# Kernel tuning notes

Measured on AMD Instinct MI355X. Metric: run time of the kernel, lower is better.

## Reference

```python
import jax, jax.numpy as jnp
import numpy as np

N = 50000       # nodes per batched graph
E = 800000      # edges per batched graph
G = 256         # graphs per batch (for max-node pooling)
VOCAB = 120     # node types == embedding vocab
D_EMB = 32
D_H = 100
D_FC = 32
MIN_TYPE = 5    # min_type_count in compute_node_pair_mmd
CAP = 25        # max_nodes_per_type (deterministic: first CAP nodes per type)
KER_MUL = 2.0   # standard multi-kernel Gaussian MMD settings
KER_NUM = 5


def setup_inputs() -> dict:
    key = jax.random.key(0)
    ks = jax.random.split(key, 16)
    ri = lambda k, sh, hi: jax.random.randint(k, sh, 0, hi, dtype=jnp.int32)
    feat = ri(ks[0], (N,), VOCAB)
    feat_src = ri(ks[1], (N,), VOCAB)
    feat_tar = ri(ks[2], (N,), VOCAB)
    edge_index = ri(ks[3], (2, E), N)
    edge_index_src = ri(ks[4], (2, E), N)
    edge_index_tar = ri(ks[5], (2, E), N)
    graph_ids = (jnp.arange(N, dtype=jnp.int32) * G) // N  # sorted, even partition
    mask = (jax.random.uniform(ks[6], (N,)) > 0.1).astype(jnp.float32)
    embed = jax.random.normal(ks[7], (VOCAB, D_EMB)) * 0.02
    gcn_w = jax.random.normal(ks[8], (D_EMB, D_H)) * (1.0 / np.sqrt(D_EMB))
    gcn_b = jnp.zeros((D_H,), jnp.float32)
    fc_w = jax.random.normal(ks[9], (D_H, D_FC)) * (1.0 / np.sqrt(D_H))
    fc_b = jnp.zeros((D_FC,), jnp.float32)
    def_w = jax.random.normal(ks[10], (D_FC, 1)) * (1.0 / np.sqrt(D_FC))
    def_b = jnp.zeros((1,), jnp.float32)
    return dict(feat=feat, feat_src=feat_src, feat_tar=feat_tar,
                edge_index=edge_index, edge_index_src=edge_index_src,
                edge_index_tar=edge_index_tar, graph_ids=graph_ids, mask=mask,
                embed=embed, gcn_w=gcn_w, gcn_b=gcn_b, fc_w=fc_w, fc_b=fc_b,
                def_w=def_w, def_b=def_b)


def _graph_conv(x, ei, w, b):
    # DGL GraphConv, norm='both': D_out^{-1/2} A^T D_in^{-1/2} X W + b (degrees clamped to 1)
    src, dst = ei[0], ei[1]
    ones = jnp.ones((ei.shape[1],), x.dtype)
    outdeg = jnp.clip(jax.ops.segment_sum(ones, src, num_segments=N), 1.0)
    indeg = jnp.clip(jax.ops.segment_sum(ones, dst, num_segments=N), 1.0)
    h = (x @ w) * (outdeg ** -0.5)[:, None]          # [N, D_H], weight first (in<=out)
    agg = jax.ops.segment_sum(h[src], dst, num_segments=N)
    return agg * (indeg ** -0.5)[:, None] + b


def _mmd(src_types, tgt_types, src_feats, tgt_feats):
    # per-type multi-kernel Gaussian MMD; deterministic cap of CAP nodes/type
    def per_type(t):
        sm = (src_types == t)
        tm = (tgt_types == t)
        s_cnt = sm.sum()
        t_cnt = tm.sum()
        sv, si = jax.lax.top_k(sm.astype(jnp.float32), CAP)  # first CAP indices of type t
        tv, ti = jax.lax.top_k(tm.astype(jnp.float32), CAP)
        X = jnp.concatenate([src_feats[si], tgt_feats[ti]], 0)      # [2C, D]
        valid = jnp.concatenate([sv, tv]) > 0                        # [2C]
        pm = valid[:, None] & valid[None, :]
        D2 = jnp.sum((X[:, None, :] - X[None, :, :]) ** 2, -1)      # [2C, 2C]
        m = jnp.minimum(s_cnt, CAP).astype(jnp.float32)
        n = jnp.minimum(t_cnt, CAP).astype(jnp.float32)
        ntot = m + n
        bw = jnp.sum(jnp.where(pm, D2, 0.0)) / jnp.maximum(ntot * ntot - ntot, 1.0)
        bw = bw / (KER_MUL ** (KER_NUM // 2))
        bws = bw * (KER_MUL ** jnp.arange(KER_NUM, dtype=jnp.float32))
        K = jnp.sum(jnp.exp(-D2[None] / jnp.maximum(bws, 1e-8)[:, None, None]), 0)
        K = jnp.where(pm, K, 0.0)
        XX = K[:CAP, :CAP].sum() / jnp.maximum(m * m, 1.0)
        YY = K[CAP:, CAP:].sum() / jnp.maximum(n * n, 1.0)
        XY = K[:CAP, CAP:].sum() / jnp.maximum(m * n, 1.0)
        loss = XX + YY - 2.0 * XY
        inc = (s_cnt >= MIN_TYPE) & (t_cnt >= MIN_TYPE)
        return jnp.where(inc, loss, 0.0), inc.astype(jnp.float32)
    losses, incs = jax.vmap(per_type)(jnp.arange(1, VOCAB, dtype=jnp.int32))  # type 0 skipped
    cnt = incs.sum()
    return jnp.where(cnt > 0, losses.sum() / jnp.maximum(cnt, 1.0), 0.0)


def reference(feat, feat_src, feat_tar, edge_index, edge_index_src, edge_index_tar,
              graph_ids, mask, embed, gcn_w, gcn_b, fc_w, fc_b, def_w, def_b):
    def process(f, ei, msk):
        x = embed[f]
        if msk is not None:
            x = x * msk[:, None]
        h = jax.nn.relu(_graph_conv(x, ei, gcn_w, gcn_b))            # node feats 'h'
        pooled = jax.ops.segment_max(h, graph_ids, num_segments=G,
                                     indices_are_sorted=True)        # dgl.max_nodes
        return h, pooled

    _, pool = process(feat, edge_index, mask)
    h_src, pool_src = process(feat_src, edge_index_src, None)
    h_tar, pool_tar = process(feat_tar, edge_index_tar, None)

    x_batch_mmd = pool @ fc_w + fc_b        # [G, 32]
    x_src_mmd = pool_src @ fc_w + fc_b
    x_tar_mmd = pool_tar @ fc_w + fc_b
    src_node_feat = h_src @ fc_w + fc_b     # [N, 32]
    tgt_node_feat = h_tar @ fc_w + fc_b
    x_loss_mmd_node = _mmd(feat_src, feat_tar, src_node_feat, tgt_node_feat)
    defect_prob = jax.nn.sigmoid(x_batch_mmd @ def_w + def_b)  # [G, 1]
    # domain_clf output is not returned by the original forward, so it is skipped here.
    return (x_batch_mmd, defect_prob, x_src_mmd, x_tar_mmd, x_loss_mmd_node)
```

## Files before the change

### kernel.cpp

```cpp
#include <hip/hip_runtime.h>
#include <hip/hip_bf16.h>

#define Nn 50000
#define Ee 800000
#define Gg 256
#define VOC 120
#define DH 100
#define CAPc 25
#define NTYPE 119
#define NCHUNK 196
#define DR 4
#define DS 32
#define DWORDS 6250
#define NBIN 391
#define EBLK 782

#define P1_T 0
#define P1_SEL 120
#define P1_BIN 512
#define P1_DEG 2858
#define P1_PCLR 3242
#define P1_SCLR 3317
#define P1_TOT 3415
#define P2_SELP 0
#define P2_BINP 240
#define P2_DMG 1413
#define P2_TOT 2585
#define P3_SELG 0
#define P3_BSC 392
#define P3_TOT 2738

__global__ __launch_bounds__(256) void prep_kernel(
        const float* __restrict__ embed, const float* __restrict__ gcn_w, float* __restrict__ Tp,
        const int* __restrict__ feat_src, const int* __restrict__ feat_tar,
        int* __restrict__ chunkcnt,
        const int* __restrict__ ei0, const int* __restrict__ ei1, const int* __restrict__ ei2,
        int* __restrict__ cntbuf, int* __restrict__ partial,
        float* __restrict__ pool, int* __restrict__ selpos, float* __restrict__ stats) {
    __shared__ int sm[DWORDS];
    int bx = blockIdx.x;
    int tid = threadIdx.x;

    if (bx < P1_SEL) {
        int t = bx - P1_T;
        if (tid < DH) {
            float acc = 0.f;
#pragma unroll
            for (int k = 0; k < 32; ++k) acc = fmaf(embed[t * 32 + k], gcn_w[k * DH + tid], acc);
            Tp[t * DH + tid] = acc;
        }
        return;
    }
    if (bx < P1_BIN) {
        int idx = bx - P1_SEL;
        int side = idx / NCHUNK, chunk = idx - side * NCHUNK;
        const int* f = side ? feat_tar : feat_src;
        if (tid < VOC) sm[tid] = 0;
        __syncthreads();
        int i = chunk * 256 + tid;
        if (i < Nn) atomicAdd(&sm[f[i]], 1);
        __syncthreads();
        if (tid < VOC) chunkcnt[(side * NCHUNK + chunk) * VOC + tid] = sm[tid];
        return;
    }
    if (bx < P1_DEG) {
        int idx = bx - P1_BIN;
        int g = idx / EBLK, blk = idx - g * EBLK;
        const int* dst = ((g == 0) ? ei0 : (g == 1) ? ei1 : ei2) + Ee;
        for (int i = tid; i < NBIN; i += 256) sm[i] = 0;
        __syncthreads();
        int e0 = (blk * 256 + tid) * 4;
        if (e0 < Ee) {
            uint4 d = *(const uint4*)&dst[e0];
            atomicAdd(&sm[d.x >> 7], 1);
            atomicAdd(&sm[d.y >> 7], 1);
            atomicAdd(&sm[d.z >> 7], 1);
            atomicAdd(&sm[d.w >> 7], 1);
        }
        __syncthreads();
        int* outp = cntbuf + ((size_t)blk * 3 + g) * NBIN;
        for (int i = tid; i < NBIN; i += 256) outp[i] = sm[i];
        return;
    }
    if (bx < P1_PCLR) {
        int idx = bx - P1_DEG;
        int g = idx / (DR * DS), rs = idx - g * (DR * DS);
        int r = rs & (DR - 1), s = rs >> 2;
        const int* ei = (g == 0) ? ei0 : (g == 1) ? ei1 : ei2;
        const uint4* a4 = (const uint4*)(ei + s * (Ee / DS));
        for (int i = tid; i < DWORDS; i += 256) sm[i] = 0;
        __syncthreads();
        unsigned base = r * (2 * DWORDS);
        for (int idx2 = tid; idx2 < (Ee / DS) / 4; idx2 += 256) {
            uint4 v = a4[idx2];
            unsigned q;
            q = v.x - base; if (q < 2 * DWORDS) atomicAdd(&sm[q >> 1], 1 << ((q & 1) * 16));
            q = v.y - base; if (q < 2 * DWORDS) atomicAdd(&sm[q >> 1], 1 << ((q & 1) * 16));
            q = v.z - base; if (q < 2 * DWORDS) atomicAdd(&sm[q >> 1], 1 << ((q & 1) * 16));
            q = v.w - base; if (q < 2 * DWORDS) atomicAdd(&sm[q >> 1], 1 << ((q & 1) * 16));
        }
        __syncthreads();
        int* outp = partial + ((size_t)(g * DR + r) * DS + s) * DWORDS;
        for (int i = tid; i < DWORDS; i += 256) outp[i] = sm[i];
        return;
    }
    if (bx < P1_SCLR) {
        int i = (bx - P1_PCLR) * 256 + tid;
        ((float4*)pool)[i] = make_float4(0.f, 0.f, 0.f, 0.f);
        return;
    }
    {
        int b = bx - P1_SCLR;
        int i = b * 256 + tid;
        if (i < 25000) ((int4*)selpos)[i] = make_int4(-1, -1, -1, -1);
        if (b == 0 && tid == 0) {
            stats[0] = 0.f;
            ((int*)stats)[1] = 0;
            ((int*)stats)[2] = 0;
        }
        return;
    }
}

__global__ __launch_bounds__(64) void prefix_kernel(const int* __restrict__ chunkcnt,
                                                    int* __restrict__ baseb,
                                                    int* __restrict__ fullcnt,
                                                    const int* __restrict__ cntbuf,
                                                    int* __restrict__ ofsbuf,
                                                    int* __restrict__ bintot,
                                                    const int* __restrict__ partial,
                                                    const int* __restrict__ feat0,
                                                    const int* __restrict__ feat_src,
                                                    const int* __restrict__ feat_tar,
                                                    const float* __restrict__ mask,
                                                    float2* __restrict__ pc) {
    int bx = blockIdx.x;
    int lane = threadIdx.x;
    if (bx < P2_BINP) {
        int side = bx / VOC, t = bx - side * VOC;
        int run = 0;
        for (int c0 = 0; c0 < NCHUNK; c0 += 64) {
            int c = c0 + lane;
            int v = (c < NCHUNK) ? chunkcnt[(side * NCHUNK + c) * VOC + t] : 0;
            int inc = v;
#pragma unroll
            for (int o = 1; o < 64; o <<= 1) {
                int u = __shfl_up(inc, o, 64);
                if (lane >= o) inc += u;
            }
            if (c < NCHUNK) baseb[(side * NCHUNK + c) * VOC + t] = run + inc - v;
            run += __shfl(inc, 63, 64);
        }
        if (lane == 0) fullcnt[side * VOC + t] = run;
        return;
    }
    if (bx < P2_DMG) {
        int pair = bx - P2_BINP;
        int g = pair / NBIN, bin = pair - g * NBIN;
        int run = 0;
        for (int c0 = 0; c0 < EBLK; c0 += 64) {
            int c = c0 + lane;
            int v = (c < EBLK) ? cntbuf[((size_t)c * 3 + g) * NBIN + bin] : 0;
            int inc = v;
#pragma unroll
            for (int o = 1; o < 64; o <<= 1) {
                int u = __shfl_up(inc, o, 64);
                if (lane >= o) inc += u;
            }
            if (c < EBLK) ofsbuf[((size_t)c * 3 + g) * NBIN + bin] = run + inc - v;
            run += __shfl(inc, 63, 64);
        }
        if (lane == 0) bintot[pair] = run;
        return;
    }
    {
        int idx = (bx - P2_DMG) * 64 + lane;
        if (idx >= 3 * DR * DWORDS) return;
        int g = idx / (DR * DWORDS);
        int rem = idx - g * (DR * DWORDS);
        int r = rem / DWORDS, w = rem - r * DWORDS;
        const int* p = partial + ((size_t)(g * DR + r) * DS) * DWORDS + w;
        int sum = 0;
#pragma unroll 8
        for (int s = 0; s < DS; ++s) sum += p[s * DWORDS];
        int c0 = sum & 0xFFFF, c1 = sum >> 16;
        int n0 = r * (2 * DWORDS) + 2 * w;
        const int* ft = (g == 0) ? feat0 : (g == 1) ? feat_src : feat_tar;
        float cf0 = rsqrtf((float)max(c0, 1));
        float cf1 = rsqrtf((float)max(c1, 1));
        if (g == 0) {
            cf0 *= mask[n0];
            cf1 *= mask[n0 + 1];
        }
        float4 v = make_float4(cf0, __int_as_float(ft[n0]), cf1, __int_as_float(ft[n0 + 1]));
        ((float4*)(pc + (size_t)g * Nn))[r * DWORDS + w] = v;
        return;
    }
}

__global__ __launch_bounds__(64) void binbase_kernel(const int* __restrict__ bintot,
                                                     int* __restrict__ binbase) {
    int g = blockIdx.x;
    int lane = threadIdx.x;
    int run = 0;
    for (int c0 = 0; c0 < NBIN; c0 += 64) {
        int c = c0 + lane;
        int v = (c < NBIN) ? bintot[g * NBIN + c] : 0;
        int inc = v;
#pragma unroll
        for (int o = 1; o < 64; o <<= 1) {
            int u = __shfl_up(inc, o, 64);
            if (lane >= o) inc += u;
        }
        if (c < NBIN) binbase[g * NBIN + c] = run + inc - v;
        run += __shfl(inc, 63, 64);
    }
}

__global__ __launch_bounds__(256) void scatter_kernel(
        const int* __restrict__ feat_src, const int* __restrict__ feat_tar,
        const int* __restrict__ baseb, int* __restrict__ selpos_src, int* __restrict__ selpos_tar,
        const int* __restrict__ ei0, const int* __restrict__ ei1, const int* __restrict__ ei2,
        const int* __restrict__ ofsbuf, const int* __restrict__ binbase,
        uint2* __restrict__ ebuf, const float2* __restrict__ pc) {
    __shared__ int sm[NBIN];
    int bx = blockIdx.x;
    int tid = threadIdx.x;

    if (bx < P3_BSC) {
        int idx = bx - P3_SELG;
        int side = idx / NCHUNK, chunk = idx - side * NCHUNK;
        const int* f = side ? feat_tar : feat_src;
        int* selpos = side ? selpos_tar : selpos_src;
        int i = chunk * 256 + tid;
        int t = (i < Nn) ? f[i] : -1;
        sm[tid] = t;
        int bv = 0;
        bool need = (t >= 1);
        if (need) {
            bv = baseb[(side * NCHUNK + chunk) * VOC + t];
            need = (bv < CAPc);
        }
        int any = __syncthreads_count((int)need);
        if (any == 0) return;
        if (need) {
            int rank = bv;
            for (int q = 0; q < 256; ++q)
                if (q < tid && sm[q] == t) rank++;
            if (rank < CAPc) selpos[i] = (t - 1) * CAPc + rank;
        }
        return;
    }
    {
        int idx = bx - P3_BSC;
        int g = idx / EBLK, blk = idx - g * EBLK;
        const int* ei = (g == 0) ? ei0 : (g == 1) ? ei1 : ei2;
        const int* ofp = ofsbuf + ((size_t)blk * 3 + g) * NBIN;
        for (int i = tid; i < NBIN; i += 256)
            sm[i] = binbase[g * NBIN + i] + ofp[i];
        __syncthreads();
        const float2* pcg = pc + (size_t)g * Nn;
        uint2* eb = ebuf + (size_t)g * Ee;
        int e0 = (blk * 256 + tid) * 4;
        if (e0 < Ee) {
            uint4 s = *(const uint4*)&ei[e0];
            uint4 d = *(const uint4*)&ei[Ee + e0];
            float2 p0 = pcg[s.x];
            float2 p1 = pcg[s.y];
            float2 p2 = pcg[s.z];
            float2 p3 = pcg[s.w];
            int p;
            p = atomicAdd(&sm[d.x >> 7], 1);
            eb[p] = make_uint2(__float_as_uint(p0.x), __float_as_int(p0.y) * 128 + (d.x & 127u));
            p = atomicAdd(&sm[d.y >> 7], 1);
            eb[p] = make_uint2(__float_as_uint(p1.x), __float_as_int(p1.y) * 128 + (d.y & 127u));
            p = atomicAdd(&sm[d.z >> 7], 1);
            eb[p] = make_uint2(__float_as_uint(p2.x), __float_as_int(p2.y) * 128 + (d.z & 127u));
            p = atomicAdd(&sm[d.w >> 7], 1);
            eb[p] = make_uint2(__float_as_uint(p3.x), __float_as_int(p3.y) * 128 + (d.w & 127u));
        }
        return;
    }
}

__global__ __launch_bounds__(256, 2) void fused_wh_kernel(const uint2* __restrict__ ebuf,
                                                          const int* __restrict__ binbase,
                                                          const int* __restrict__ bintot,
                                                          const float* __restrict__ Tp,
                                                          const int* __restrict__ selposall,
                                                          float* __restrict__ h_sel,
                                                          const float* __restrict__ gcn_b,
                                                          float* __restrict__ pool) {
    __shared__ float Wl[VOC * 128];
    __shared__ int cnt[128];
    int g = blockIdx.y, bin = blockIdx.x;
    int tid = threadIdx.x;

    float4* Wl4 = (float4*)Wl;
#pragma unroll
    for (int i = 0; i < 15; ++i) Wl4[tid + i * 256] = make_float4(0.f, 0.f, 0.f, 0.f);
    if (tid < 128) cnt[tid] = 0;
    __syncthreads();

    int base = binbase[g * NBIN + bin];
    int n = bintot[g * NBIN + bin];
    const uint2* eb = ebuf + (size_t)g * Ee + base;
    for (int i = tid; i < n; i += 256) {
        uint2 e = eb[i];
        atomicAdd(&Wl[e.y], __uint_as_float(e.x));
        atomicAdd(&cnt[e.y & 127u], 1);
    }
    __syncthreads();

    int lane = tid & 63, wv = tid >> 6;
    int chcol = __builtin_amdgcn_readfirstlane(wv) * 25;
    const float* Tc = Tp + chcol;
    int r0 = bin * 128;
    int nr = min(128, Nn - r0);
    float accA[25], accB[25];
#pragma unroll
    for (int j = 0; j < 25; ++j) { accA[j] = 0.f; accB[j] = 0.f; }

    for (int t0 = 0; t0 < VOC; t0 += 8) {
        float wA8[8], wB8[8];
#pragma unroll
        for (int u = 0; u < 8; ++u) {
            wA8[u] = Wl[(t0 + u) * 128 + lane];
            wB8[u] = Wl[(t0 + u) * 128 + lane + 64];
        }
#pragma unroll
        for (int u = 0; u < 8; ++u) {
            const float* tr = Tc + (t0 + u) * DH;
#pragma unroll
            for (int j = 0; j < 25; ++j) {
                float tv = tr[j];
                accA[j] = fmaf(wA8[u], tv, accA[j]);
                accB[j] = fmaf(wB8[u], tv, accB[j]);
            }
        }
    }

    int rA = lane, rB = lane + 64;
    bool vA = rA < nr, vB = rB < nr;
    float rsA = vA ? rsqrtf((float)max(cnt[rA], 1)) : 0.f;
    float rsB = vB ? rsqrtf((float)max(cnt[rB], 1)) : 0.f;
    int growA = r0 + rA, growB = r0 + rB;
    int seg0 = (r0 * Gg) / Nn;
    int segA = (growA * Gg) / Nn, segB = (growB * Gg) / Nn;
    float bb[25];
#pragma unroll
    for (int j = 0; j < 25; ++j) bb[j] = gcn_b[wv * 25 + j];

    float v0[25], v1[25];
#pragma unroll
    for (int j = 0; j < 25; ++j) {
        float hA = vA ? fmaxf(fmaf(accA[j], rsA, bb[j]), 0.f) : 0.f;
        float hB = vB ? fmaxf(fmaf(accB[j], rsB, bb[j]), 0.f) : 0.f;
        accA[j] = hA;
        accB[j] = hB;
        v0[j] = fmaxf((vA && segA == seg0) ? hA : 0.f, (vB && segB == seg0) ? hB : 0.f);
        v1[j] = fmaxf((vA && segA != seg0) ? hA : 0.f, (vB && segB != seg0) ? hB : 0.f);
    }
#pragma unroll
    for (int m = 1; m < 64; m <<= 1) {
#pragma unroll
        for (int j = 0; j < 25; ++j) {
            v0[j] = fmaxf(v0[j], __shfl_xor(v0[j], m, 64));
            v1[j] = fmaxf(v1[j], __shfl_xor(v1[j], m, 64));
        }
    }
    if (lane == 0) {
        float* poolg = pool + g * (Gg * DH) + seg0 * DH + wv * 25;
        for (int j = 0; j < 25; ++j) atomicMax((int*)&poolg[j], __float_as_int(v0[j]));
        int segLast = ((r0 + nr - 1) * Gg) / Nn;
        if (segLast != seg0)
            for (int j = 0; j < 25; ++j) atomicMax((int*)&poolg[DH + j], __float_as_int(v1[j]));
    }

    if (g > 0) {
        const int* selpos = selposall + (size_t)(g - 1) * Nn;
        float* hs = h_sel + (size_t)(g == 2 ? NTYPE * CAPc * DH : 0);
        int spA = vA ? selpos[growA] : -1;
        int spB = vB ? selpos[growB] : -1;
        if (spA >= 0) {
            float* d = hs + (size_t)spA * DH + wv * 25;
            for (int j = 0; j < 25; ++j) d[j] = accA[j];
        }
        if (spB >= 0) {
            float* d = hs + (size_t)spB * DH + wv * 25;
            for (int j = 0; j < 25; ++j) d[j] = accB[j];
        }
    }
}

__global__ __launch_bounds__(256) void post_kernel(const float* __restrict__ pool,
                                                   const float* __restrict__ fc_w,
                                                   const float* __restrict__ fc_b,
                                                   const float* __restrict__ def_w,
                                                   const float* __restrict__ def_b,
                                                   float* __restrict__ out,
                                                   const float* __restrict__ h_sel,
                                                   const int* __restrict__ fullcnt,
                                                   float* __restrict__ X) {
    __shared__ float smf[DH * 32];
    int bx = blockIdx.x;
    int tid = threadIdx.x;
    if (bx < Gg) {
        int g = bx;
        if (tid < 96) {
            int p = tid >> 5, j = tid & 31;
            float acc = fc_b[j];
            const float* pr = pool + p * (Gg * DH) + g * DH;
#pragma unroll 4
            for (int k = 0; k < DH; ++k) acc = fmaf(pr[k], fc_w[k * 32 + j], acc);
            int off = (p == 0) ? 0 : (p == 1 ? 8448 : 16640);
            out[off + g * 32 + j] = acc;
            if (p == 0) smf[j] = acc;
        }
        __syncthreads();
        if (tid < 32) {
            float v = smf[tid] * def_w[tid];
            for (int o = 16; o; o >>= 1) v += __shfl_down(v, o, 64);
            if (tid == 0) out[8192 + g] = 1.f / (1.f + expf(-(v + def_b[0])));
        }
        return;
    }
    {
        int t = bx - Gg;
        for (int i = tid; i < DH * 32; i += 256) smf[i] = fc_w[i];
        __syncthreads();
        int cs = min(fullcnt[t + 1], CAPc);
        int ct = min(fullcnt[VOC + t + 1], CAPc);
        int j = tid & 31, rg = tid >> 5;
        for (int r = rg; r < 2 * CAPc; r += 8) {
            int side = r / CAPc, rr = r % CAPc;
            int cnt = side ? ct : cs;
            float acc = 0.f;
            if (rr < cnt) {
                const float* hr = h_sel + ((size_t)side * NTYPE * CAPc + (size_t)t * CAPc + rr) * DH;
                acc = fc_b[j];
#pragma unroll 4
                for (int k = 0; k < DH; ++k) acc = fmaf(hr[k], smf[k * 32 + j], acc);
            }
            X[(size_t)t * 1600 + r * 32 + j] = acc;
        }
        return;
    }
}

__device__ __forceinline__ float block_reduce256(float v, float* red, int tid) {
    __syncthreads();
    red[tid] = v;
    __syncthreads();
    for (int s = 128; s > 0; s >>= 1) {
        if (tid < s) red[tid] += red[tid + s];
        __syncthreads();
    }
    return red[0];
}

__global__ __launch_bounds__(256) void mmd_kernel(const float* __restrict__ X,
                                                  const int* __restrict__ fullcnt,
                                                  float* __restrict__ stats,
                                                  float* __restrict__ out) {
    int t = blockIdx.x;
    __shared__ float Xs[50 * 32];
    __shared__ float D2[50 * 50];
    __shared__ float red[256];
    int tid = threadIdx.x;
    for (int i = tid; i < 1600; i += 256) Xs[i] = X[(size_t)t * 1600 + i];
    __syncthreads();
    int scF = fullcnt[t + 1];
    int tcF = fullcnt[VOC + t + 1];
    int m = min(scF, CAPc), n2 = min(tcF, CAPc);
    float bwpart = 0.f;
    for (int idx = tid; idx < 2500; idx += 256) {
        int i = idx / 50, j = idx % 50;
        float d = 0.f;
#pragma unroll
        for (int k = 0; k < 32; ++k) {
            float df = Xs[i * 32 + k] - Xs[j * 32 + k];
            d = fmaf(df, df, d);
        }
        D2[idx] = d;
        bool vi = (i < CAPc) ? (i < m) : (i - CAPc < n2);
        bool vj = (j < CAPc) ? (j < m) : (j - CAPc < n2);
        if (vi && vj) bwpart += d;
    }
    float bwsum = block_reduce256(bwpart, red, tid);
    float ntot = (float)(m + n2);
    float bw = bwsum / fmaxf(ntot * ntot - ntot, 1.f) * 0.25f;
    float bws[5];
#pragma unroll
    for (int k = 0; k < 5; ++k) bws[k] = fmaxf(bw * (float)(1 << k), 1e-8f);
    float xx = 0.f, yy = 0.f, xy = 0.f;
    for (int idx = tid; idx < 2500; idx += 256) {
        int i = idx / 50, j = idx % 50;
        bool vi = (i < CAPc) ? (i < m) : (i - CAPc < n2);
        bool vj = (j < CAPc) ? (j < m) : (j - CAPc < n2);
        if (!(vi && vj)) continue;
        float d = D2[idx];
        float kv = 0.f;
#pragma unroll
        for (int k = 0; k < 5; ++k) kv += expf(-d / bws[k]);
        if (i < CAPc && j < CAPc) xx += kv;
        else if (i >= CAPc && j >= CAPc) yy += kv;
        else if (i < CAPc) xy += kv;
    }
    float rxx = block_reduce256(xx, red, tid);
    float ryy = block_reduce256(yy, red, tid);
    float rxy = block_reduce256(xy, red, tid);
    if (tid == 0) {
        float fm = (float)m, fn = (float)n2;
        float XX = rxx / fmaxf(fm * fm, 1.f);
        float YY = ryy / fmaxf(fn * fn, 1.f);
        float XY = rxy / fmaxf(fm * fn, 1.f);
        float loss = XX + YY - 2.f * XY;
        int inc = (scF >= 5 && tcF >= 5) ? 1 : 0;
        atomicAdd(&stats[0], inc ? loss : 0.f);
        atomicAdd((int*)&stats[1], inc);
        __threadfence();
        int old = atomicAdd((int*)&stats[2], 1);
        if (old == NTYPE - 1) {
            float s = atomicAdd(&stats[0], 0.f);
            int c = atomicAdd((int*)&stats[1], 0);
            out[24832] = (c > 0) ? s / (float)max(c, 1) : 0.f;
        }
    }
}

extern "C" void kernel_launch(void* const* d_in, const int* in_sizes, int n_in,
                              void* d_out, int out_size, void* d_ws, size_t ws_size,
                              hipStream_t stream) {
    const int* feat = (const int*)d_in[0];
    const int* feat_src = (const int*)d_in[1];
    const int* feat_tar = (const int*)d_in[2];
    const int* ei0 = (const int*)d_in[3];
    const int* ei1 = (const int*)d_in[4];
    const int* ei2 = (const int*)d_in[5];
    const float* mask = (const float*)d_in[7];
    const float* embed = (const float*)d_in[8];
    const float* gcn_w = (const float*)d_in[9];
    const float* gcn_b = (const float*)d_in[10];
    const float* fc_w = (const float*)d_in[11];
    const float* fc_b = (const float*)d_in[12];
    const float* def_w = (const float*)d_in[13];
    const float* def_b = (const float*)d_in[14];
    float* out = (float*)d_out;

    char* wsb = (char*)d_ws;
    int* partial = (int*)(wsb + 0);
    float* Tp = (float*)(wsb + 9600000);
    float* pool = (float*)(wsb + 9660000);
    float2* pc = (float2*)(wsb + 9967200);
    int* selpos = (int*)(wsb + 11167200);
    float* h_sel = (float*)(wsb + 11567200);
    int* fullcnt = (int*)(wsb + 13947200);
    float* X = (float*)(wsb + 13948160);
    float* stats = (float*)(wsb + 14709760);
    int* chunkcnt = (int*)(wsb + 14710720);
    int* baseb = (int*)(wsb + 14898880);
    int* cntbuf = (int*)(wsb + 15087040);
    int* ofsbuf = (int*)(wsb + 18756200);
    int* bintot = (int*)(wsb + 22425400);
    int* binbase = (int*)(wsb + 22430400);
    uint2* ebuf = (uint2*)(wsb + 22435200);

    prep_kernel<<<P1_TOT, 256, 0, stream>>>(embed, gcn_w, Tp, feat_src, feat_tar, chunkcnt,
                                            ei0, ei1, ei2, cntbuf, partial, pool, selpos, stats);
    prefix_kernel<<<P2_TOT, 64, 0, stream>>>(chunkcnt, baseb, fullcnt, cntbuf, ofsbuf, bintot,
                                             partial, feat, feat_src, feat_tar, mask, pc);
    binbase_kernel<<<3, 64, 0, stream>>>(bintot, binbase);
    scatter_kernel<<<P3_TOT, 256, 0, stream>>>(feat_src, feat_tar, baseb, selpos, selpos + Nn,
                                               ei0, ei1, ei2, ofsbuf, binbase, ebuf, pc);
    fused_wh_kernel<<<dim3(NBIN, 3), 256, 0, stream>>>(ebuf, binbase, bintot, Tp, selpos,
                                                       h_sel, gcn_b, pool);
    post_kernel<<<Gg + NTYPE, 256, 0, stream>>>(pool, fc_w, fc_b, def_w, def_b, out, h_sel,
                                                fullcnt, X);
    mmd_kernel<<<NTYPE, 256, 0, stream>>>(X, fullcnt, stats, out);
}
```

Baseline: 215.0 us.

## Make fused_wh persistent and fold MMD kernel into post kernel

Turns fused_wh_kernel into a persistent grid of 512 blocks that loop over the 3*391 (graph, bin) jobs, hoisting the bias load out of the loop. The separate mmd_kernel is merged into post_kernel's per-type blocks, so the projected features stay in shared memory and no longer go through the global X buffer. The aim is to save one kernel launch and a global round trip, and to reduce block scheduling overhead. In exchange, the persistent loop can leave the jobs unevenly spread across blocks, and post_kernel now uses more shared memory per block.

```diff
diff --git a/kernel.cpp b/kernel.cpp
--- a/kernel.cpp
+++ b/kernel.cpp
@@ -14,6 +14,7 @@
 #define DWORDS 6250
 #define NBIN 391
 #define EBLK 782
+#define FWH_GRID 512
 
 #define P1_T 0
 #define P1_SEL 120
@@ -293,104 +294,119 @@
                                                           float* __restrict__ pool) {
     __shared__ float Wl[VOC * 128];
     __shared__ int cnt[128];
-    int g = blockIdx.y, bin = blockIdx.x;
     int tid = threadIdx.x;
-
-    float4* Wl4 = (float4*)Wl;
-#pragma unroll
-    for (int i = 0; i < 15; ++i) Wl4[tid + i * 256] = make_float4(0.f, 0.f, 0.f, 0.f);
-    if (tid < 128) cnt[tid] = 0;
-    __syncthreads();
-
-    int base = binbase[g * NBIN + bin];
-    int n = bintot[g * NBIN + bin];
-    const uint2* eb = ebuf + (size_t)g * Ee + base;
-    for (int i = tid; i < n; i += 256) {
-        uint2 e = eb[i];
-        atomicAdd(&Wl[e.y], __uint_as_float(e.x));
-        atomicAdd(&cnt[e.y & 127u], 1);
-    }
-    __syncthreads();
-
     int lane = tid & 63, wv = tid >> 6;
     int chcol = __builtin_amdgcn_readfirstlane(wv) * 25;
     const float* Tc = Tp + chcol;
-    int r0 = bin * 128;
-    int nr = min(128, Nn - r0);
-    float accA[25], accB[25];
-#pragma unroll
-    for (int j = 0; j < 25; ++j) { accA[j] = 0.f; accB[j] = 0.f; }
-
-    for (int t0 = 0; t0 < VOC; t0 += 8) {
-        float wA8[8], wB8[8];
-#pragma unroll
-        for (int u = 0; u < 8; ++u) {
-            wA8[u] = Wl[(t0 + u) * 128 + lane];
-            wB8[u] = Wl[(t0 + u) * 128 + lane + 64];
-        }
-#pragma unroll
-        for (int u = 0; u < 8; ++u) {
-            const float* tr = Tc + (t0 + u) * DH;
+    float bb[25];
+#pragma unroll
+    for (int j = 0; j < 25; ++j) bb[j] = gcn_b[wv * 25 + j];
+
+    for (int job = blockIdx.x; job < 3 * NBIN; job += FWH_GRID) {
+        int g = job / NBIN, bin = job - g * NBIN;
+
+        float4* Wl4 = (float4*)Wl;
+#pragma unroll
+        for (int i = 0; i < 15; ++i) Wl4[tid + i * 256] = make_float4(0.f, 0.f, 0.f, 0.f);
+        if (tid < 128) cnt[tid] = 0;
+        __syncthreads();
+
+        int base = binbase[g * NBIN + bin];
+        int n = bintot[g * NBIN + bin];
+        const uint2* eb = ebuf + (size_t)g * Ee + base;
+        for (int i = tid; i < n; i += 256) {
+            uint2 e = eb[i];
+            atomicAdd(&Wl[e.y], __uint_as_float(e.x));
+            atomicAdd(&cnt[e.y & 127u], 1);
+        }
+        __syncthreads();
+
+        int r0 = bin * 128;
+        int nr = min(128, Nn - r0);
+        float accA[25], accB[25];
+#pragma unroll
+        for (int j = 0; j < 25; ++j) { accA[j] = 0.f; accB[j] = 0.f; }
+
+        for (int t0 = 0; t0 < VOC; t0 += 8) {
+            float wA8[8], wB8[8];
+#pragma unroll
+            for (int u = 0; u < 8; ++u) {
+                wA8[u] = Wl[(t0 + u) * 128 + lane];
+                wB8[u] = Wl[(t0 + u) * 128 + lane + 64];
+            }
+#pragma unroll
+            for (int u = 0; u < 8; ++u) {
+                const float* tr = Tc + (t0 + u) * DH;
+#pragma unroll
+                for (int j = 0; j < 25; ++j) {
+                    float tv = tr[j];
+                    accA[j] = fmaf(wA8[u], tv, accA[j]);
+                    accB[j] = fmaf(wB8[u], tv, accB[j]);
+                }
+            }
+        }
+
+        int rA = lane, rB = lane + 64;
+        bool vA = rA < nr, vB = rB < nr;
+        float rsA = vA ? rsqrtf((float)max(cnt[rA], 1)) : 0.f;
+        float rsB = vB ? rsqrtf((float)max(cnt[rB], 1)) : 0.f;
+        int growA = r0 + rA, growB = r0 + rB;
+        int seg0 = (r0 * Gg) / Nn;
+        int segA = (growA * Gg) / Nn, segB = (growB * Gg) / Nn;
+
+        float v0[25], v1[25];
+#pragma unroll
+        for (int j = 0; j < 25; ++j) {
+            float hA = vA ? fmaxf(fmaf(accA[j], rsA, bb[j]), 0.f) : 0.f;
+            float hB = vB ? fmaxf(fmaf(accB[j], rsB, bb[j]), 0.f) : 0.f;
+            accA[j] = hA;
+            accB[j] = hB;
+            v0[j] = fmaxf((vA && segA == seg0) ? hA : 0.f, (vB && segB == seg0) ? hB : 0.f);
+            v1[j] = fmaxf((vA && segA != seg0) ? hA : 0.f, (vB && segB != seg0) ? hB : 0.f);
+        }
+#pragma unroll
+        for (int m = 1; m < 64; m <<= 1) {
 #pragma unroll
             for (int j = 0; j < 25; ++j) {
-                float tv = tr[j];
-                accA[j] = fmaf(wA8[u], tv, accA[j]);
-                accB[j] = fmaf(wB8[u], tv, accB[j]);
-            }
-        }
-    }
-
-    int rA = lane, rB = lane + 64;
-    bool vA = rA < nr, vB = rB < nr;
-    float rsA = vA ? rsqrtf((float)max(cnt[rA], 1)) : 0.f;
-    float rsB = vB ? rsqrtf((float)max(cnt[rB], 1)) : 0.f;
-    int growA = r0 + rA, growB = r0 + rB;
-    int seg0 = (r0 * Gg) / Nn;
-    int segA = (growA * Gg) / Nn, segB = (growB * Gg) / Nn;
-    float bb[25];
-#pragma unroll
-    for (int j = 0; j < 25; ++j) bb[j] = gcn_b[wv * 25 + j];
-
-    float v0[25], v1[25];
-#pragma unroll
-    for (int j = 0; j < 25; ++j) {
-        float hA = vA ? fmaxf(fmaf(accA[j], rsA, bb[j]), 0.f) : 0.f;
-        float hB = vB ? fmaxf(fmaf(accB[j], rsB, bb[j]), 0.f) : 0.f;
-        accA[j] = hA;
-        accB[j] = hB;
-        v0[j] = fmaxf((vA && segA == seg0) ? hA : 0.f, (vB && segB == seg0) ? hB : 0.f);
-        v1[j] = fmaxf((vA && segA != seg0) ? hA : 0.f, (vB && segB != seg0) ? hB : 0.f);
-    }
-#pragma unroll
-    for (int m = 1; m < 64; m <<= 1) {
-#pragma unroll
-        for (int j = 0; j < 25; ++j) {
-            v0[j] = fmaxf(v0[j], __shfl_xor(v0[j], m, 64));
-            v1[j] = fmaxf(v1[j], __shfl_xor(v1[j], m, 64));
-        }
-    }
-    if (lane == 0) {
-        float* poolg = pool + g * (Gg * DH) + seg0 * DH + wv * 25;
-        for (int j = 0; j < 25; ++j) atomicMax((int*)&poolg[j], __float_as_int(v0[j]));
-        int segLast = ((r0 + nr - 1) * Gg) / Nn;
-        if (segLast != seg0)
-            for (int j = 0; j < 25; ++j) atomicMax((int*)&poolg[DH + j], __float_as_int(v1[j]));
-    }
-
-    if (g > 0) {
-        const int* selpos = selposall + (size_t)(g - 1) * Nn;
-        float* hs = h_sel + (size_t)(g == 2 ? NTYPE * CAPc * DH : 0);
-        int spA = vA ? selpos[growA] : -1;
-        int spB = vB ? selpos[growB] : -1;
-        if (spA >= 0) {
-            float* d = hs + (size_t)spA * DH + wv * 25;
-            for (int j = 0; j < 25; ++j) d[j] = accA[j];
-        }
-        if (spB >= 0) {
-            float* d = hs + (size_t)spB * DH + wv * 25;
-            for (int j = 0; j < 25; ++j) d[j] = accB[j];
-        }
-    }
+                v0[j] = fmaxf(v0[j], __shfl_xor(v0[j], m, 64));
+                v1[j] = fmaxf(v1[j], __shfl_xor(v1[j], m, 64));
+            }
+        }
+        if (lane == 0) {
+            float* poolg = pool + g * (Gg * DH) + seg0 * DH + wv * 25;
+            for (int j = 0; j < 25; ++j) atomicMax((int*)&poolg[j], __float_as_int(v0[j]));
+            int segLast = ((r0 + nr - 1) * Gg) / Nn;
+            if (segLast != seg0)
+                for (int j = 0; j < 25; ++j) atomicMax((int*)&poolg[DH + j], __float_as_int(v1[j]));
+        }
+
+        if (g > 0) {
+            const int* selpos = selposall + (size_t)(g - 1) * Nn;
+            float* hs = h_sel + (size_t)(g == 2 ? NTYPE * CAPc * DH : 0);
+            int spA = vA ? selpos[growA] : -1;
+            int spB = vB ? selpos[growB] : -1;
+            if (spA >= 0) {
+                float* d = hs + (size_t)spA * DH + wv * 25;
+                for (int j = 0; j < 25; ++j) d[j] = accA[j];
+            }
+            if (spB >= 0) {
+                float* d = hs + (size_t)spB * DH + wv * 25;
+                for (int j = 0; j < 25; ++j) d[j] = accB[j];
+            }
+        }
+        __syncthreads();
+    }
+}
+
+__device__ __forceinline__ float block_reduce256(float v, float* red, int tid) {
+    __syncthreads();
+    red[tid] = v;
+    __syncthreads();
+    for (int s = 128; s > 0; s >>= 1) {
+        if (tid < s) red[tid] += red[tid + s];
+        __syncthreads();
+    }
+    return red[0];
 }
 
 __global__ __launch_bounds__(256) void post_kernel(const float* __restrict__ pool,
@@ -401,8 +417,11 @@
                                                    float* __restrict__ out,
                                                    const float* __restrict__ h_sel,
                                                    const int* __restrict__ fullcnt,
-                                                   float* __restrict__ X) {
+                                                   float* __restrict__ stats) {
     __shared__ float smf[DH * 32];
+    __shared__ float Xs[50 * 32];
+    __shared__ float D2[50 * 50];
+    __shared__ float red[256];
     int bx = blockIdx.x;
     int tid = threadIdx.x;
     if (bx < Gg) {
@@ -429,103 +448,81 @@
         int t = bx - Gg;
         for (int i = tid; i < DH * 32; i += 256) smf[i] = fc_w[i];
         __syncthreads();
-        int cs = min(fullcnt[t + 1], CAPc);
-        int ct = min(fullcnt[VOC + t + 1], CAPc);
-        int j = tid & 31, rg = tid >> 5;
-        for (int r = rg; r < 2 * CAPc; r += 8) {
-            int side = r / CAPc, rr = r % CAPc;
-            int cnt = side ? ct : cs;
-            float acc = 0.f;
-            if (rr < cnt) {
-                const float* hr = h_sel + ((size_t)side * NTYPE * CAPc + (size_t)t * CAPc + rr) * DH;
-                acc = fc_b[j];
+        int scF = fullcnt[t + 1];
+        int tcF = fullcnt[VOC + t + 1];
+        int m = min(scF, CAPc), n2 = min(tcF, CAPc);
+        {
+            int j = tid & 31, rg = tid >> 5;
+            for (int r = rg; r < 2 * CAPc; r += 8) {
+                int side = r / CAPc, rr = r % CAPc;
+                int cnt = side ? n2 : m;
+                float acc = 0.f;
+                if (rr < cnt) {
+                    const float* hr =
+                        h_sel + ((size_t)side * NTYPE * CAPc + (size_t)t * CAPc + rr) * DH;
+                    acc = fc_b[j];
 #pragma unroll 4
-                for (int k = 0; k < DH; ++k) acc = fmaf(hr[k], smf[k * 32 + j], acc);
-            }
-            X[(size_t)t * 1600 + r * 32 + j] = acc;
-        }
-        return;
-    }
-}
-
-__device__ __forceinline__ float block_reduce256(float v, float* red, int tid) {
-    __syncthreads();
-    red[tid] = v;
-    __syncthreads();
-    for (int s = 128; s > 0; s >>= 1) {
-        if (tid < s) red[tid] += red[tid + s];
-        __syncthreads();
-    }
-    return red[0];
-}
-
-__global__ __launch_bounds__(256) void mmd_kernel(const float* __restrict__ X,
-                                                  const int* __restrict__ fullcnt,
-                                                  float* __restrict__ stats,
-                                                  float* __restrict__ out) {
-    int t = blockIdx.x;
-    __shared__ float Xs[50 * 32];
-    __shared__ float D2[50 * 50];
-    __shared__ float red[256];
-    int tid = threadIdx.x;
-    for (int i = tid; i < 1600; i += 256) Xs[i] = X[(size_t)t * 1600 + i];
-    __syncthreads();
-    int scF = fullcnt[t + 1];
-    int tcF = fullcnt[VOC + t + 1];
-    int m = min(scF, CAPc), n2 = min(tcF, CAPc);
-    float bwpart = 0.f;
-    for (int idx = tid; idx < 2500; idx += 256) {
-        int i = idx / 50, j = idx % 50;
-        float d = 0.f;
-#pragma unroll
-        for (int k = 0; k < 32; ++k) {
-            float df = Xs[i * 32 + k] - Xs[j * 32 + k];
-            d = fmaf(df, df, d);
-        }
-        D2[idx] = d;
-        bool vi = (i < CAPc) ? (i < m) : (i - CAPc < n2);
-        bool vj = (j < CAPc) ? (j < m) : (j - CAPc < n2);
-        if (vi && vj) bwpart += d;
-    }
-    float bwsum = block_reduce256(bwpart, red, tid);
-    float ntot = (float)(m + n2);
-    float bw = bwsum / fmaxf(ntot * ntot - ntot, 1.f) * 0.25f;
-    float bws[5];
-#pragma unroll
-    for (int k = 0; k < 5; ++k) bws[k] = fmaxf(bw * (float)(1 << k), 1e-8f);
-    float xx = 0.f, yy = 0.f, xy = 0.f;
-    for (int idx = tid; idx < 2500; idx += 256) {
-        int i = idx / 50, j = idx % 50;
-        bool vi = (i < CAPc) ? (i < m) : (i - CAPc < n2);
-        bool vj = (j < CAPc) ? (j < m) : (j - CAPc < n2);
-        if (!(vi && vj)) continue;
-        float d = D2[idx];
-        float kv = 0.f;
-#pragma unroll
-        for (int k = 0; k < 5; ++k) kv += expf(-d / bws[k]);
-        if (i < CAPc && j < CAPc) xx += kv;
-        else if (i >= CAPc && j >= CAPc) yy += kv;
-        else if (i < CAPc) xy += kv;
-    }
-    float rxx = block_reduce256(xx, red, tid);
-    float ryy = block_reduce256(yy, red, tid);
-    float rxy = block_reduce256(xy, red, tid);
-    if (tid == 0) {
-        float fm = (float)m, fn = (float)n2;
-        float XX = rxx / fmaxf(fm * fm, 1.f);
-        float YY = ryy / fmaxf(fn * fn, 1.f);
-        float XY = rxy / fmaxf(fm * fn, 1.f);
-        float loss = XX + YY - 2.f * XY;
-        int inc = (scF >= 5 && tcF >= 5) ? 1 : 0;
-        atomicAdd(&stats[0], inc ? loss : 0.f);
-        atomicAdd((int*)&stats[1], inc);
-        __threadfence();
-        int old = atomicAdd((int*)&stats[2], 1);
-        if (old == NTYPE - 1) {
-            float s = atomicAdd(&stats[0], 0.f);
-            int c = atomicAdd((int*)&stats[1], 0);
-            out[24832] = (c > 0) ? s / (float)max(c, 1) : 0.f;
-        }
+                    for (int k = 0; k < DH; ++k) acc = fmaf(hr[k], smf[k * 32 + j], acc);
+                }
+                Xs[r * 32 + j] = acc;
+            }
+        }
+        __syncthreads();
+        float bwpart = 0.f;
+        for (int idx = tid; idx < 2500; idx += 256) {
+            int i = idx / 50, j = idx % 50;
+            float d = 0.f;
+#pragma unroll
+            for (int k = 0; k < 32; ++k) {
+                float df = Xs[i * 32 + k] - Xs[j * 32 + k];
+                d = fmaf(df, df, d);
+            }
+            D2[idx] = d;
+            bool vi = (i < CAPc) ? (i < m) : (i - CAPc < n2);
+            bool vj = (j < CAPc) ? (j < m) : (j - CAPc < n2);
+            if (vi && vj) bwpart += d;
+        }
+        float bwsum = block_reduce256(bwpart, red, tid);
+        float ntot = (float)(m + n2);
+        float bw = bwsum / fmaxf(ntot * ntot - ntot, 1.f) * 0.25f;
+        float bws[5];
+#pragma unroll
+        for (int k = 0; k < 5; ++k) bws[k] = fmaxf(bw * (float)(1 << k), 1e-8f);
+        float xx = 0.f, yy = 0.f, xy = 0.f;
+        for (int idx = tid; idx < 2500; idx += 256) {
+            int i = idx / 50, j = idx % 50;
+            bool vi = (i < CAPc) ? (i < m) : (i - CAPc < n2);
+            bool vj = (j < CAPc) ? (j < m) : (j - CAPc < n2);
+            if (!(vi && vj)) continue;
+            float d = D2[idx];
+            float kv = 0.f;
+#pragma unroll
+            for (int k = 0; k < 5; ++k) kv += expf(-d / bws[k]);
+            if (i < CAPc && j < CAPc) xx += kv;
+            else if (i >= CAPc && j >= CAPc) yy += kv;
+            else if (i < CAPc) xy += kv;
+        }
+        float rxx = block_reduce256(xx, red, tid);
+        float ryy = block_reduce256(yy, red, tid);
+        float rxy = block_reduce256(xy, red, tid);
+        if (tid == 0) {
+            float fm = (float)m, fn = (float)n2;
+            float XX = rxx / fmaxf(fm * fm, 1.f);
+            float YY = ryy / fmaxf(fn * fn, 1.f);
+            float XY = rxy / fmaxf(fm * fn, 1.f);
+            float loss = XX + YY - 2.f * XY;
+            int inc = (scF >= 5 && tcF >= 5) ? 1 : 0;
+            atomicAdd(&stats[0], inc ? loss : 0.f);
+            atomicAdd((int*)&stats[1], inc);
+            __threadfence();
+            int old = atomicAdd((int*)&stats[2], 1);
+            if (old == NTYPE - 1) {
+                float s = atomicAdd(&stats[0], 0.f);
+                int c = atomicAdd((int*)&stats[1], 0);
+                out[24832] = (c > 0) ? s / (float)max(c, 1) : 0.f;
+            }
+        }
+        return;
     }
 }
 
@@ -556,7 +553,6 @@
     int* selpos = (int*)(wsb + 11167200);
     float* h_sel = (float*)(wsb + 11567200);
     int* fullcnt = (int*)(wsb + 13947200);
-    float* X = (float*)(wsb + 13948160);
     float* stats = (float*)(wsb + 14709760);
     int* chunkcnt = (int*)(wsb + 14710720);
     int* baseb = (int*)(wsb + 14898880);
@@ -573,9 +569,8 @@
     binbase_kernel<<<3, 64, 0, stream>>>(bintot, binbase);
     scatter_kernel<<<P3_TOT, 256, 0, stream>>>(feat_src, feat_tar, baseb, selpos, selpos + Nn,
                                                ei0, ei1, ei2, ofsbuf, binbase, ebuf, pc);
-    fused_wh_kernel<<<dim3(NBIN, 3), 256, 0, stream>>>(ebuf, binbase, bintot, Tp, selpos,
-                                                       h_sel, gcn_b, pool);
+    fused_wh_kernel<<<FWH_GRID, 256, 0, stream>>>(ebuf, binbase, bintot, Tp, selpos,
+                                                  h_sel, gcn_b, pool);
     post_kernel<<<Gg + NTYPE, 256, 0, stream>>>(pool, fc_w, fc_b, def_w, def_b, out, h_sel,
-                                                fullcnt, X);
-    mmd_kernel<<<NTYPE, 256, 0, stream>>>(X, fullcnt, stats, out);
-}
+                                                fullcnt, stats);
+}
```

Result: faster. 205.7 us (-4.3%).
